# Performance work log

Measured on AMD Instinct MI355X. Metric: run time of the kernel, lower is better.

Reference implementation:

```python
import jax, jax.numpy as jnp
import numpy as np

K = 20
BN_SCALE = 1.0 / np.sqrt(1.0 + 1e-5)  # BN at init: running_mean=0, running_var=1


def _graph_feature(x, k):
    # x: (B, N, C) point features -> (B, N, k, 2C) edge features
    sq = jnp.sum(x * x, axis=-1)  # (B, N)
    # negative squared distance: larger == closer (matches torch topk on -dist)
    d = 2.0 * jnp.einsum('bnc,bmc->bnm', x, x) - sq[:, :, None] - sq[:, None, :]
    idx = jax.lax.top_k(d, k)[1]  # (B, N, k), self included as nearest
    nbr = jax.vmap(lambda pts, i: pts[i])(x, idx)  # (B, N, k, C) gather
    ctr = jnp.broadcast_to(x[:, :, None, :], nbr.shape)
    return jnp.concatenate([nbr - ctr, ctr], axis=-1)


def _edge_conv(e, W, g, b):
    # 1x1 Conv2d (no bias) + BatchNorm(init stats) + LeakyReLU(0.2) + max over k
    y = jnp.einsum('bnkc,oc->bnko', e, W)
    y = jax.nn.leaky_relu(y * (g * BN_SCALE) + b, 0.2)
    return jnp.max(y, axis=2)  # (B, N, O)


def setup_inputs() -> dict:
    key = jax.random.key(0)
    ks = jax.random.split(key, 12)
    B, N = 4, 1024
    dims_in = [6, 128, 256, 512]
    dims_out = [64, 128, 256, 512]
    inp = {'x': jax.random.normal(ks[0], (B, N, 3), dtype=jnp.float32)}
    for i, (ci, co) in enumerate(zip(dims_in, dims_out), start=1):
        inp[f'W{i}'] = jax.random.normal(ks[i], (co, ci), dtype=jnp.float32) * (1.0 / np.sqrt(ci))
        inp[f'g{i}'] = jnp.ones((co,), dtype=jnp.float32)
        inp[f'b{i}'] = jnp.zeros((co,), dtype=jnp.float32)
    inp['W5'] = jax.random.normal(ks[5], (512, 960), dtype=jnp.float32) * (1.0 / np.sqrt(960.0))
    inp['g5'] = jnp.ones((512,), dtype=jnp.float32)
    inp['b5'] = jnp.zeros((512,), dtype=jnp.float32)
    inp['We'] = jax.random.normal(ks[6], (256, 512), dtype=jnp.float32) * (1.0 / np.sqrt(512.0))
    return inp


def reference(x, W1, g1, b1, W2, g2, b2, W3, g3, b3, W4, g4, b4, W5, g5, b5, We):
    x1 = _edge_conv(_graph_feature(x, K), W1, g1, b1)   # (B, N, 64)
    x2 = _edge_conv(_graph_feature(x1, K), W2, g2, b2)  # (B, N, 128)
    x3 = _edge_conv(_graph_feature(x2, K), W3, g3, b3)  # (B, N, 256)
    x4 = _edge_conv(_graph_feature(x3, K), W4, g4, b4)  # (B, N, 512)
    xc = jnp.concatenate([x1, x2, x3, x4], axis=-1)     # (B, N, 960)
    y = jnp.einsum('bnc,oc->bno', xc, W5)               # conv5 (1x1 Conv1d)
    y = jax.nn.leaky_relu(y * (g5 * BN_SCALE) + b5, 0.2)
    feat = jnp.max(y, axis=1)                           # (B, 512) global max-pool
    return feat @ We.T                                  # (B, num_features)
```

## Files before the change

### kernel.cpp

```cpp
#include <hip/hip_runtime.h>
#include <hip/hip_bf16.h>
#include <math.h>

typedef __hip_bfloat16 bf16;
typedef __bf16 v8bf __attribute__((ext_vector_type(8)));
typedef float v4f __attribute__((ext_vector_type(4)));

#define BN_SCALE 0.9999950000374997f
#define NPTS 1024
#define NB 4
#define TW 40

__device__ __forceinline__ float b2f(bf16 v) { return __bfloat162float(v); }
__device__ __forceinline__ bf16 f2b(float v) { return __float2bfloat16(v); }
__device__ __forceinline__ float ldw(const void* p, size_t i, int isf) {
    return isf ? ((const float*)p)[i] : b2f(((const bf16*)p)[i]);
}
__device__ __forceinline__ unsigned ordf(float f) {
    unsigned u = __float_as_uint(f);
    return (u & 0x80000000u) ? ~u : (u | 0x80000000u);
}
__device__ __forceinline__ float iordf(unsigned u) {
    return (u & 0x80000000u) ? __uint_as_float(u ^ 0x80000000u) : __uint_as_float(~u);
}

__device__ __forceinline__ int detect_isf(const void* xraw, int* cnt) {
    const unsigned short* u = (const unsigned short*)xraw;
    int t = threadIdx.x, c = 0;
    for (int i = t; i < 512; i += 256) {
        unsigned short v = u[i];
        int e = (v >> 7) & 0xFF;
        int m = v & 0x7F;
        if (e == 0xFF || e >= 141 || (e == 0 && m != 0)) c++;
    }
    cnt[t] = c;
    __syncthreads();
    for (int off = 128; off > 0; off >>= 1) {
        if (t < off) cnt[t] += cnt[t + off];
        __syncthreads();
    }
    int isf = (cnt[0] > 30) ? 1 : 0;
    __syncthreads();
    return isf;
}

__global__ void k_prep(const void* __restrict__ W1, const void* __restrict__ W2,
                       const void* __restrict__ W3, const void* __restrict__ W4,
                       const void* __restrict__ W5, const void* __restrict__ x,
                       bf16* __restrict__ Whi, bf16* __restrict__ Wlo,
                       bf16* __restrict__ xph, bf16* __restrict__ xpl, float* __restrict__ sq,
                       int* __restrict__ flag, unsigned* __restrict__ pooledU) {
    __shared__ int cnt[256];
    int isf = detect_isf(x, cnt);
    if (blockIdx.x == 0) {
        if (threadIdx.x == 0) *flag = isf;
        for (int i = threadIdx.x; i < 2048; i += 256) pooledU[i] = 0u;
    }
    int idx = blockIdx.x * 256 + threadIdx.x;
    if (idx < 839680) {
        const void* src; int C, O, Kpad, two, local;
        if (idx < 4096)        { src = W1; C = 3;   O = 64;  Kpad = 32;  two = 1; local = idx; }
        else if (idx < 20480)  { src = W2; C = 64;  O = 128; Kpad = 64;  two = 1; local = idx - 4096; }
        else if (idx < 86016)  { src = W3; C = 128; O = 256; Kpad = 128; two = 1; local = idx - 20480; }
        else if (idx < 348160) { src = W4; C = 256; O = 512; Kpad = 256; two = 1; local = idx - 86016; }
        else                   { src = W5; C = 960; O = 512; Kpad = 960; two = 0; local = idx - 348160; }
        int r = local / Kpad, c = local % Kpad;
        float wv = 0.f;
        if (c < C) {
            size_t off;
            if (two) off = (r < O) ? (size_t)r * 2 * C + c : (size_t)(r - O) * 2 * C + C + c;
            else     off = (size_t)r * C + c;
            wv = ldw(src, off, isf);
        }
        bf16 h = f2b(wv);
        Whi[idx] = h;
        Wlo[idx] = f2b(wv - b2f(h));
    } else if (idx < 843776) {
        int p = idx - 839680;
        int z = p >> 10, n = p & 1023;
        bf16* ph = xph + (size_t)z * NPTS * 32;
        bf16* pl = xpl + (size_t)z * NPTS * 32;
        float s = 0.f;
        for (int c = 0; c < 32; c++) {
            float v = (c < 3) ? ldw(x, (size_t)z * NPTS * 3 + n * 3 + c, isf) : 0.f;
            bf16 h = f2b(v);
            ph[n * 32 + c] = h;
            pl[n * 32 + c] = f2b(v - b2f(h));
            s += v * v;
        }
        sq[z * NPTS + n] = s;
    }
}

__device__ __forceinline__ void fillA(bf16* dst, const bf16* srcRowBase, int ld) {
    int t = threadIdx.x; int r = t >> 2; int kq = (t & 3) << 3;
    *(float4*)(dst + r * TW + kq) = *(const float4*)(srcRowBase + (size_t)r * ld + kq);
}
__device__ __forceinline__ v8bf ldfrag(const bf16* tile, int sub, int l) {
    return *(const v8bf*)(tile + (size_t)(sub * 16 + (l & 15)) * TW + ((l >> 4) << 3));
}

__global__ __launch_bounds__(256) void k_layer_a(const bf16* __restrict__ Xhi, const bf16* __restrict__ Xlo,
                                                 int ld, int Kpad, size_t xstride,
                                                 const bf16* __restrict__ Whi, const bf16* __restrict__ Wlo,
                                                 int O, const float* __restrict__ sqg,
                                                 float* __restrict__ Dg, float* __restrict__ Pg,
                                                 const int* __restrict__ flag) {
    int i = blockIdx.x;
    int z = (i >> 1) & 3;
    int bi = ((i >> 3) << 1) | (i & 1);
    const bf16* Xh = Xhi + (size_t)z * xstride;
    const bf16* Xl = Xlo + (size_t)z * xstride;
    __shared__ alignas(16) bf16 Ah[64 * TW], Al[64 * TW], Bh[64 * TW], Bl[64 * TW];
    int w = threadIdx.x >> 6, l = threadIdx.x & 63;
    int quad = l >> 4, col = l & 15;
    v4f zero = {0.f, 0.f, 0.f, 0.f};
    v4f acc[4] = {zero, zero, zero, zero};

    if (bi < 136) {
        int bx = 0;
        while ((((bx + 1) * (bx + 2)) >> 1) <= bi) bx++;
        int by = bi - ((bx * (bx + 1)) >> 1);
        const float* sq = sqg + z * NPTS;
        float* D = Dg + (size_t)z * NPTS * NPTS;
        int n0 = by * 64, m0 = bx * 64;
        for (int k0 = 0; k0 < Kpad; k0 += 32) {
            __syncthreads();
            fillA(Ah, Xh + (size_t)n0 * ld + k0, ld);
            fillA(Bh, Xh + (size_t)m0 * ld + k0, ld);
            fillA(Al, Xl + (size_t)n0 * ld + k0, ld);
            fillA(Bl, Xl + (size_t)m0 * ld + k0, ld);
            __syncthreads();
            v8bf ah = ldfrag(Ah, w, l);
            v8bf al = ldfrag(Al, w, l);
#pragma unroll
            for (int nt = 0; nt < 4; nt++) {
                v8bf bh = ldfrag(Bh, nt, l);
                v8bf bl = ldfrag(Bl, nt, l);
                acc[nt] = __builtin_amdgcn_mfma_f32_16x16x32_bf16(ah, bh, acc[nt], 0, 0, 0);
                acc[nt] = __builtin_amdgcn_mfma_f32_16x16x32_bf16(ah, bl, acc[nt], 0, 0, 0);
                acc[nt] = __builtin_amdgcn_mfma_f32_16x16x32_bf16(al, bh, acc[nt], 0, 0, 0);
            }
        }
        int nb = n0 + 16 * w + quad * 4;
        float sm[4];
#pragma unroll
        for (int nt = 0; nt < 4; nt++) sm[nt] = sq[m0 + nt * 16 + col];
#pragma unroll
        for (int r = 0; r < 4; r++) {
            float sn = sq[nb + r];
#pragma unroll
            for (int nt = 0; nt < 4; nt++) {
                float d = 2.f * acc[nt][r] - sn - sm[nt];
                int m = m0 + nt * 16 + col;
                D[(size_t)(nb + r) * NPTS + m] = d;
                if (bx != by) D[(size_t)m * NPTS + nb + r] = d;
            }
        }
    } else {
        int isf = *flag;
        int nTilesO = (2 * O) >> 6;
        int s = bi - 136;
        int n0 = (s % nTilesO) * 64;
        int m0 = (s / nTilesO) * 64;
        int N2 = 2 * O;
        float* P = Pg + (size_t)z * NPTS * N2;
        for (int k0 = 0; k0 < Kpad; k0 += 32) {
            __syncthreads();
            fillA(Ah, Xh + (size_t)m0 * ld + k0, ld);
            fillA(Al, Xl + (size_t)m0 * ld + k0, ld);
            fillA(Bh, Whi + (size_t)n0 * Kpad + k0, Kpad);
            if (isf) fillA(Bl, Wlo + (size_t)n0 * Kpad + k0, Kpad);
            __syncthreads();
            v8bf ah = ldfrag(Ah, w, l);
            v8bf al = ldfrag(Al, w, l);
#pragma unroll
            for (int nt = 0; nt < 4; nt++) {
                v8bf bh = ldfrag(Bh, nt, l);
                acc[nt] = __builtin_amdgcn_mfma_f32_16x16x32_bf16(ah, bh, acc[nt], 0, 0, 0);
                acc[nt] = __builtin_amdgcn_mfma_f32_16x16x32_bf16(al, bh, acc[nt], 0, 0, 0);
                if (isf) {
                    v8bf bl = ldfrag(Bl, nt, l);
                    acc[nt] = __builtin_amdgcn_mfma_f32_16x16x32_bf16(ah, bl, acc[nt], 0, 0, 0);
                }
            }
        }
        int rb = m0 + 16 * w + quad * 4;
#pragma unroll
        for (int r = 0; r < 4; r++)
#pragma unroll
            for (int nt = 0; nt < 4; nt++)
                P[(size_t)(rb + r) * N2 + n0 + nt * 16 + col] = acc[nt][r];
    }
}

__global__ __launch_bounds__(256) void k_layer_b(const float* __restrict__ Dg, const float* __restrict__ Pg,
                                                 const void* __restrict__ g, const void* __restrict__ bias,
                                                 int O, bf16* __restrict__ xhOut, bf16* __restrict__ xlOut,
                                                 float* __restrict__ sqOut, int writeSq,
                                                 const int* __restrict__ flag) {
    __shared__ int ids[4][20];
    __shared__ float sqP[4][8];
    int isf = *flag;
    int i = blockIdx.x;
    int z = (i >> 1) & 3;
    int local = ((i >> 3) << 1) | (i & 1);
    int tid = threadIdx.x;
    int wq = tid >> 6, l = tid & 63;
    int row = local * 4 + wq;

    {
        const float* Dr = Dg + (size_t)z * NPTS * NPTS + (size_t)row * NPTS;
        float v[16];
#pragma unroll
        for (int jj = 0; jj < 4; jj++) {
            float4 f4 = *(const float4*)(Dr + jj * 256 + l * 4);
            v[jj * 4 + 0] = f4.x; v[jj * 4 + 1] = f4.y;
            v[jj * 4 + 2] = f4.z; v[jj * 4 + 3] = f4.w;
        }
        for (int s = 0; s < 20; s++) {
            float bv = v[0]; int bj = 0;
#pragma unroll
            for (int j = 1; j < 16; j++)
                if (v[j] > bv) { bv = v[j]; bj = j; }
            int bi = (bj >> 2) * 256 + l * 4 + (bj & 3);
#pragma unroll
            for (int off = 1; off < 64; off <<= 1) {
                float ov = __shfl_xor(bv, off);
                int   oi = __shfl_xor(bi, off);
                if (ov > bv || (ov == bv && oi < bi)) { bv = ov; bi = oi; }
            }
            if (l == 0) ids[wq][s] = bi;
            if (((bi >> 2) & 63) == l) {
                int ej = (bi >> 8) * 4 + (bi & 3);
#pragma unroll
                for (int j = 0; j < 16; j++)
                    if (j == ej) v[j] = -__builtin_inff();
            }
        }
    }
    __syncthreads();

    int N2 = 2 * O;
    const float* P = Pg + (size_t)z * NPTS * N2;
    for (int it = tid; it < 4 * O; it += 256) {
        int r = it / O, o = it % O;
        int n = local * 4 + r;
        float tv = P[(size_t)n * N2 + O + o] - P[(size_t)n * N2 + o];
        float scl = ldw(g, o, isf) * BN_SCALE;
        float bb = ldw(bias, o, isf);
        float acc = -__builtin_inff();
        for (int j = 0; j < 20; j++) {
            int m = ids[r][j];
            float v = P[(size_t)m * N2 + o] + tv;
            float z2 = v * scl + bb;
            z2 = z2 > 0.f ? z2 : 0.2f * z2;
            acc = fmaxf(acc, z2);
        }
        bf16 hi = f2b(acc);
        bf16 lo = f2b(acc - b2f(hi));
        xhOut[(size_t)z * NPTS * 960 + (size_t)n * 960 + o] = hi;
        xlOut[(size_t)z * NPTS * 960 + (size_t)n * 960 + o] = lo;
        if (writeSq) {
            float xv = b2f(hi) + b2f(lo);
            float s = xv * xv;
#pragma unroll
            for (int off = 32; off > 0; off >>= 1) s += __shfl_down(s, off);
            if (l == 0) sqP[r][o >> 6] = s;
        }
    }
    if (writeSq) {
        __syncthreads();
        if (tid < 4) {
            int nc = O >> 6;
            float tot = 0.f;
            for (int c = 0; c < nc; c++) tot += sqP[tid][c];
            sqOut[z * NPTS + local * 4 + tid] = tot;
        }
    }
}

__global__ __launch_bounds__(256) void k_conv5(const bf16* __restrict__ Xhi, const bf16* __restrict__ Xlo,
                                               const bf16* __restrict__ Whi, const bf16* __restrict__ Wlo,
                                               const void* __restrict__ g, const void* __restrict__ bias,
                                               unsigned* __restrict__ pooledU,
                                               const int* __restrict__ flag) {
    int isf = *flag;
    int i = blockIdx.x;
    int z = (i >> 1) & 3;
    int wi = ((i >> 3) << 1) | (i & 1);
    int o0 = (wi & 7) * 64, m0 = (wi >> 3) * 64;
    const bf16* Xh = Xhi + (size_t)z * NPTS * 960;
    const bf16* Xl = Xlo + (size_t)z * NPTS * 960;
    __shared__ alignas(16) bf16 Ah[64 * TW], Al[64 * TW], Bh[64 * TW], Bl[64 * TW];
    __shared__ float red[4][4][16];
    int w = threadIdx.x >> 6, l = threadIdx.x & 63;
    v4f zero = {0.f, 0.f, 0.f, 0.f};
    v4f acc[4] = {zero, zero, zero, zero};
    for (int k0 = 0; k0 < 960; k0 += 32) {
        __syncthreads();
        fillA(Ah, Xh + (size_t)m0 * 960 + k0, 960);
        fillA(Al, Xl + (size_t)m0 * 960 + k0, 960);
        fillA(Bh, Whi + (size_t)o0 * 960 + k0, 960);
        if (isf) fillA(Bl, Wlo + (size_t)o0 * 960 + k0, 960);
        __syncthreads();
        v8bf ah = ldfrag(Ah, w, l);
        v8bf al = ldfrag(Al, w, l);
#pragma unroll
        for (int nt = 0; nt < 4; nt++) {
            v8bf bh = ldfrag(Bh, nt, l);
            acc[nt] = __builtin_amdgcn_mfma_f32_16x16x32_bf16(ah, bh, acc[nt], 0, 0, 0);
            acc[nt] = __builtin_amdgcn_mfma_f32_16x16x32_bf16(al, bh, acc[nt], 0, 0, 0);
            if (isf) {
                v8bf bl = ldfrag(Bl, nt, l);
                acc[nt] = __builtin_amdgcn_mfma_f32_16x16x32_bf16(ah, bl, acc[nt], 0, 0, 0);
            }
        }
    }
    int quad = l >> 4, col = l & 15;
#pragma unroll
    for (int nt = 0; nt < 4; nt++) {
        int o = o0 + nt * 16 + col;
        float scl = ldw(g, o, isf) * BN_SCALE;
        float bi = ldw(bias, o, isf);
        float ym = -__builtin_inff();
#pragma unroll
        for (int r = 0; r < 4; r++) {
            float v = acc[nt][r] * scl + bi;
            v = v > 0.f ? v : 0.2f * v;
            ym = fmaxf(ym, v);
        }
        ym = fmaxf(ym, __shfl_down(ym, 32));
        ym = fmaxf(ym, __shfl_down(ym, 16));
        if (quad == 0) red[w][nt][col] = ym;
    }
    __syncthreads();
    if (threadIdx.x < 64) {
        int nt = threadIdx.x >> 4, c = threadIdx.x & 15;
        float m = fmaxf(fmaxf(red[0][nt][c], red[1][nt][c]), fmaxf(red[2][nt][c], red[3][nt][c]));
        atomicMax(&pooledU[z * 512 + o0 + nt * 16 + c], ordf(m));
    }
}

__global__ void k_final(const unsigned* __restrict__ pooledU, const void* __restrict__ We,
                        void* __restrict__ out, const int* __restrict__ flag) {
    __shared__ float p[512];
    int isf = *flag;
    int b = blockIdx.x >> 2, fb = blockIdx.x & 3;
    int t = threadIdx.x, w = t >> 6, l = t & 63;
    for (int i = t; i < 512; i += 256) p[i] = iordf(pooledU[b * 512 + i]);
    __syncthreads();
    for (int it = 0; it < 16; it++) {
        int f = fb * 64 + w * 16 + it;
        float s = 0.f;
        size_t base = (size_t)f * 512 + l * 8;
#pragma unroll
        for (int j = 0; j < 8; j++) s += p[l * 8 + j] * ldw(We, base + j, isf);
#pragma unroll
        for (int off = 32; off > 0; off >>= 1) s += __shfl_down(s, off);
        if (l == 0) {
            if (isf) ((float*)out)[b * 256 + f] = s;
            else     ((bf16*)out)[b * 256 + f] = f2b(s);
        }
    }
}

extern "C" void kernel_launch(void* const* d_in, const int* in_sizes, int n_in,
                              void* d_out, int out_size, void* d_ws, size_t ws_size,
                              hipStream_t stream) {
    const void* x  = d_in[0];
    const void* Wl[4] = { d_in[1], d_in[4], d_in[7], d_in[10] };
    const void* gl[4] = { d_in[2], d_in[5], d_in[8], d_in[11] };
    const void* bl[4] = { d_in[3], d_in[6], d_in[9], d_in[12] };
    const void* W5 = d_in[13];
    const void* g5 = d_in[14];
    const void* b5 = d_in[15];
    const void* We = d_in[16];

    char* base = (char*)d_ws;
    bf16*     xc_hi   = (bf16*)(base);
    bf16*     xc_lo   = (bf16*)(base + 7864320);
    bf16*     xpadh   = (bf16*)(base + 15728640);
    bf16*     xpadl   = (bf16*)(base + 15990784);
    float*    Dbuf    = (float*)(base + 16252928);
    float*    Pbuf    = (float*)(base + 33030144);
    bf16*     Whi     = (bf16*)(base + 49807360);
    bf16*     Wlo     = (bf16*)(base + 51486720);
    unsigned* pooledU = (unsigned*)(base + 53493760);
    float*    sq      = (float*)(base + 53501952);
    int*      flag    = (int*)(base + 53518336);

    const int Kpad[4]   = { 32, 64, 128, 256 };
    const int Os[4]     = { 64, 128, 256, 512 };
    const int Woff[5]   = { 0, 4096, 20480, 86016, 348160 };
    const int colIn[4]  = { 0, 0, 64, 192 };
    const int colOut[4] = { 0, 64, 192, 448 };

    k_prep<<<3296, 256, 0, stream>>>(Wl[0], Wl[1], Wl[2], Wl[3], W5, x,
                                     Whi, Wlo, xpadh, xpadl, sq, flag, pooledU);

    for (int l = 0; l < 4; l++) {
        int O = Os[l];
        int nTilesO = (2 * O) >> 6;
        int nBlk = 136 + 16 * nTilesO;
        const bf16* Xh = (l == 0) ? xpadh : (xc_hi + colIn[l]);
        const bf16* Xl = (l == 0) ? xpadl : (xc_lo + colIn[l]);
        int ld = (l == 0) ? 32 : 960;
        size_t xstr = (l == 0) ? (size_t)NPTS * 32 : (size_t)NPTS * 960;
        k_layer_a<<<nBlk * NB, 256, 0, stream>>>(
            Xh, Xl, ld, Kpad[l], xstr, Whi + Woff[l], Wlo + Woff[l], O, sq, Dbuf, Pbuf, flag);
        k_layer_b<<<NPTS * NB / 4, 256, 0, stream>>>(
            Dbuf, Pbuf, gl[l], bl[l], O, xc_hi + colOut[l], xc_lo + colOut[l], sq, l < 3, flag);
    }
    k_conv5<<<512, 256, 0, stream>>>(xc_hi, xc_lo, Whi + Woff[4], Wlo + Woff[4],
                                     g5, b5, pooledU, flag);
    k_final<<<16, 256, 0, stream>>>(pooledU, We, d_out, flag);
}
```

Before: 341.6 us.

## Enlarge GEMM tiles to 128x128 with 2x2 warp layout and 4x4 MFMA subtiles

The distance, projection and conv5 GEMM kernels move from 64x64 to 128x128 block tiles, with each wave computing a 64x64 subtile as 4x4 MFMA fragments. The aim is more reuse of each shared-memory fragment load and fewer global loads per FLOP. Grid sizes drop accordingly: the symmetric distance triangle goes from 136 to 36 tiles and conv5 from 512 to 128 blocks. In exchange, accumulator registers grow fourfold and far fewer blocks are launched, which may leave many of the GPU's CUs idle and lower occupancy.

```diff
diff --git a/kernel.cpp b/kernel.cpp
--- a/kernel.cpp
+++ b/kernel.cpp
@@ -92,11 +92,13 @@
     }
 }
 
-__device__ __forceinline__ void fillA(bf16* dst, const bf16* srcRowBase, int ld) {
-    int t = threadIdx.x; int r = t >> 2; int kq = (t & 3) << 3;
-    *(float4*)(dst + r * TW + kq) = *(const float4*)(srcRowBase + (size_t)r * ld + kq);
-}
-__device__ __forceinline__ v8bf ldfrag(const bf16* tile, int sub, int l) {
+__device__ __forceinline__ void fill128(bf16* dst, const bf16* src, int ld) {
+    int t = threadIdx.x;
+    int r = t >> 2, kq = (t & 3) << 3;
+    *(float4*)(dst + r * TW + kq) = *(const float4*)(src + (size_t)r * ld + kq);
+    *(float4*)(dst + (r + 64) * TW + kq) = *(const float4*)(src + (size_t)(r + 64) * ld + kq);
+}
+__device__ __forceinline__ v8bf ldf(const bf16* tile, int sub, int l) {
     return *(const v8bf*)(tile + (size_t)(sub * 16 + (l & 15)) * TW + ((l >> 4) << 3));
 }
 
@@ -111,86 +113,114 @@
     int bi = ((i >> 3) << 1) | (i & 1);
     const bf16* Xh = Xhi + (size_t)z * xstride;
     const bf16* Xl = Xlo + (size_t)z * xstride;
-    __shared__ alignas(16) bf16 Ah[64 * TW], Al[64 * TW], Bh[64 * TW], Bl[64 * TW];
+    __shared__ alignas(16) bf16 Ah[128 * TW], Al[128 * TW], Bh[128 * TW], Bl[128 * TW];
     int w = threadIdx.x >> 6, l = threadIdx.x & 63;
+    int wr = w >> 1, wc = w & 1;
     int quad = l >> 4, col = l & 15;
     v4f zero = {0.f, 0.f, 0.f, 0.f};
-    v4f acc[4] = {zero, zero, zero, zero};
-
-    if (bi < 136) {
+    v4f acc[4][4] = {{zero, zero, zero, zero}, {zero, zero, zero, zero},
+                     {zero, zero, zero, zero}, {zero, zero, zero, zero}};
+
+    if (bi < 36) {
         int bx = 0;
         while ((((bx + 1) * (bx + 2)) >> 1) <= bi) bx++;
         int by = bi - ((bx * (bx + 1)) >> 1);
         const float* sq = sqg + z * NPTS;
         float* D = Dg + (size_t)z * NPTS * NPTS;
-        int n0 = by * 64, m0 = bx * 64;
+        int n0 = by * 128, m0 = bx * 128;
         for (int k0 = 0; k0 < Kpad; k0 += 32) {
             __syncthreads();
-            fillA(Ah, Xh + (size_t)n0 * ld + k0, ld);
-            fillA(Bh, Xh + (size_t)m0 * ld + k0, ld);
-            fillA(Al, Xl + (size_t)n0 * ld + k0, ld);
-            fillA(Bl, Xl + (size_t)m0 * ld + k0, ld);
+            fill128(Ah, Xh + (size_t)n0 * ld + k0, ld);
+            fill128(Bh, Xh + (size_t)m0 * ld + k0, ld);
+            fill128(Al, Xl + (size_t)n0 * ld + k0, ld);
+            fill128(Bl, Xl + (size_t)m0 * ld + k0, ld);
             __syncthreads();
-            v8bf ah = ldfrag(Ah, w, l);
-            v8bf al = ldfrag(Al, w, l);
-#pragma unroll
-            for (int nt = 0; nt < 4; nt++) {
-                v8bf bh = ldfrag(Bh, nt, l);
-                v8bf bl = ldfrag(Bl, nt, l);
-                acc[nt] = __builtin_amdgcn_mfma_f32_16x16x32_bf16(ah, bh, acc[nt], 0, 0, 0);
-                acc[nt] = __builtin_amdgcn_mfma_f32_16x16x32_bf16(ah, bl, acc[nt], 0, 0, 0);
-                acc[nt] = __builtin_amdgcn_mfma_f32_16x16x32_bf16(al, bh, acc[nt], 0, 0, 0);
-            }
-        }
-        int nb = n0 + 16 * w + quad * 4;
+            v8bf ah[4], al[4];
+#pragma unroll
+            for (int mi = 0; mi < 4; mi++) {
+                ah[mi] = ldf(Ah, wr * 4 + mi, l);
+                al[mi] = ldf(Al, wr * 4 + mi, l);
+            }
+#pragma unroll
+            for (int ni = 0; ni < 4; ni++) {
+                v8bf bh = ldf(Bh, wc * 4 + ni, l);
+                v8bf bl = ldf(Bl, wc * 4 + ni, l);
+#pragma unroll
+                for (int mi = 0; mi < 4; mi++) {
+                    acc[mi][ni] = __builtin_amdgcn_mfma_f32_16x16x32_bf16(ah[mi], bh, acc[mi][ni], 0, 0, 0);
+                    acc[mi][ni] = __builtin_amdgcn_mfma_f32_16x16x32_bf16(ah[mi], bl, acc[mi][ni], 0, 0, 0);
+                    acc[mi][ni] = __builtin_amdgcn_mfma_f32_16x16x32_bf16(al[mi], bh, acc[mi][ni], 0, 0, 0);
+                }
+            }
+        }
+        int rb = n0 + wr * 64 + quad * 4;
+        int cb = m0 + wc * 64 + col;
         float sm[4];
 #pragma unroll
-        for (int nt = 0; nt < 4; nt++) sm[nt] = sq[m0 + nt * 16 + col];
-#pragma unroll
-        for (int r = 0; r < 4; r++) {
-            float sn = sq[nb + r];
-#pragma unroll
-            for (int nt = 0; nt < 4; nt++) {
-                float d = 2.f * acc[nt][r] - sn - sm[nt];
-                int m = m0 + nt * 16 + col;
-                D[(size_t)(nb + r) * NPTS + m] = d;
-                if (bx != by) D[(size_t)m * NPTS + nb + r] = d;
+        for (int ni = 0; ni < 4; ni++) sm[ni] = sq[cb + ni * 16];
+#pragma unroll
+        for (int mi = 0; mi < 4; mi++) {
+#pragma unroll
+            for (int r = 0; r < 4; r++) {
+                int row = rb + mi * 16 + r;
+                float sn = sq[row];
+#pragma unroll
+                for (int ni = 0; ni < 4; ni++) {
+                    float d = 2.f * acc[mi][ni][r] - sn - sm[ni];
+                    int c = cb + ni * 16;
+                    D[(size_t)row * NPTS + c] = d;
+                    if (bx != by) D[(size_t)c * NPTS + row] = d;
+                }
             }
         }
     } else {
         int isf = *flag;
-        int nTilesO = (2 * O) >> 6;
-        int s = bi - 136;
-        int n0 = (s % nTilesO) * 64;
-        int m0 = (s / nTilesO) * 64;
+        int nCol = (2 * O) >> 7;
+        int s = bi - 36;
+        int n0 = (s % nCol) * 128;
+        int m0 = (s / nCol) * 128;
         int N2 = 2 * O;
         float* P = Pg + (size_t)z * NPTS * N2;
         for (int k0 = 0; k0 < Kpad; k0 += 32) {
             __syncthreads();
-            fillA(Ah, Xh + (size_t)m0 * ld + k0, ld);
-            fillA(Al, Xl + (size_t)m0 * ld + k0, ld);
-            fillA(Bh, Whi + (size_t)n0 * Kpad + k0, Kpad);
-            if (isf) fillA(Bl, Wlo + (size_t)n0 * Kpad + k0, Kpad);
+            fill128(Ah, Xh + (size_t)m0 * ld + k0, ld);
+            fill128(Al, Xl + (size_t)m0 * ld + k0, ld);
+            fill128(Bh, Whi + (size_t)n0 * Kpad + k0, Kpad);
+            if (isf) fill128(Bl, Wlo + (size_t)n0 * Kpad + k0, Kpad);
             __syncthreads();
-            v8bf ah = ldfrag(Ah, w, l);
-            v8bf al = ldfrag(Al, w, l);
-#pragma unroll
-            for (int nt = 0; nt < 4; nt++) {
-                v8bf bh = ldfrag(Bh, nt, l);
-                acc[nt] = __builtin_amdgcn_mfma_f32_16x16x32_bf16(ah, bh, acc[nt], 0, 0, 0);
-                acc[nt] = __builtin_amdgcn_mfma_f32_16x16x32_bf16(al, bh, acc[nt], 0, 0, 0);
+            v8bf ah[4], al[4];
+#pragma unroll
+            for (int mi = 0; mi < 4; mi++) {
+                ah[mi] = ldf(Ah, wr * 4 + mi, l);
+                al[mi] = ldf(Al, wr * 4 + mi, l);
+            }
+#pragma unroll
+            for (int ni = 0; ni < 4; ni++) {
+                v8bf bh = ldf(Bh, wc * 4 + ni, l);
+#pragma unroll
+                for (int mi = 0; mi < 4; mi++) {
+                    acc[mi][ni] = __builtin_amdgcn_mfma_f32_16x16x32_bf16(ah[mi], bh, acc[mi][ni], 0, 0, 0);
+                    acc[mi][ni] = __builtin_amdgcn_mfma_f32_16x16x32_bf16(al[mi], bh, acc[mi][ni], 0, 0, 0);
+                }
                 if (isf) {
-                    v8bf bl = ldfrag(Bl, nt, l);
-                    acc[nt] = __builtin_amdgcn_mfma_f32_16x16x32_bf16(ah, bl, acc[nt], 0, 0, 0);
+                    v8bf bl = ldf(Bl, wc * 4 + ni, l);
+#pragma unroll
+                    for (int mi = 0; mi < 4; mi++)
+                        acc[mi][ni] = __builtin_amdgcn_mfma_f32_16x16x32_bf16(ah[mi], bl, acc[mi][ni], 0, 0, 0);
                 }
             }
         }
-        int rb = m0 + 16 * w + quad * 4;
-#pragma unroll
-        for (int r = 0; r < 4; r++)
-#pragma unroll
-            for (int nt = 0; nt < 4; nt++)
-                P[(size_t)(rb + r) * N2 + n0 + nt * 16 + col] = acc[nt][r];
+        int rb = m0 + wr * 64 + quad * 4;
+        int cb = n0 + wc * 64 + col;
+#pragma unroll
+        for (int mi = 0; mi < 4; mi++)
+#pragma unroll
+            for (int r = 0; r < 4; r++) {
+                int row = rb + mi * 16 + r;
+#pragma unroll
+                for (int ni = 0; ni < 4; ni++)
+                    P[(size_t)row * N2 + cb + ni * 16] = acc[mi][ni][r];
+            }
     }
 }
 
@@ -289,56 +319,69 @@
     int i = blockIdx.x;
     int z = (i >> 1) & 3;
     int wi = ((i >> 3) << 1) | (i & 1);
-    int o0 = (wi & 7) * 64, m0 = (wi >> 3) * 64;
+    int o0 = (wi & 3) * 128, m0 = (wi >> 2) * 128;
     const bf16* Xh = Xhi + (size_t)z * NPTS * 960;
     const bf16* Xl = Xlo + (size_t)z * NPTS * 960;
-    __shared__ alignas(16) bf16 Ah[64 * TW], Al[64 * TW], Bh[64 * TW], Bl[64 * TW];
+    __shared__ alignas(16) bf16 Ah[128 * TW], Al[128 * TW], Bh[128 * TW], Bl[128 * TW];
     __shared__ float red[4][4][16];
     int w = threadIdx.x >> 6, l = threadIdx.x & 63;
+    int wr = w >> 1, wc = w & 1;
+    int quad = l >> 4, col = l & 15;
     v4f zero = {0.f, 0.f, 0.f, 0.f};
-    v4f acc[4] = {zero, zero, zero, zero};
+    v4f acc[4][4] = {{zero, zero, zero, zero}, {zero, zero, zero, zero},
+                     {zero, zero, zero, zero}, {zero, zero, zero, zero}};
     for (int k0 = 0; k0 < 960; k0 += 32) {
         __syncthreads();
-        fillA(Ah, Xh + (size_t)m0 * 960 + k0, 960);
-        fillA(Al, Xl + (size_t)m0 * 960 + k0, 960);
-        fillA(Bh, Whi + (size_t)o0 * 960 + k0, 960);
-        if (isf) fillA(Bl, Wlo + (size_t)o0 * 960 + k0, 960);
+        fill128(Ah, Xh + (size_t)m0 * 960 + k0, 960);
+        fill128(Al, Xl + (size_t)m0 * 960 + k0, 960);
+        fill128(Bh, Whi + (size_t)o0 * 960 + k0, 960);
+        if (isf) fill128(Bl, Wlo + (size_t)o0 * 960 + k0, 960);
         __syncthreads();
-        v8bf ah = ldfrag(Ah, w, l);
-        v8bf al = ldfrag(Al, w, l);
-#pragma unroll
-        for (int nt = 0; nt < 4; nt++) {
-            v8bf bh = ldfrag(Bh, nt, l);
-            acc[nt] = __builtin_amdgcn_mfma_f32_16x16x32_bf16(ah, bh, acc[nt], 0, 0, 0);
-            acc[nt] = __builtin_amdgcn_mfma_f32_16x16x32_bf16(al, bh, acc[nt], 0, 0, 0);
+        v8bf ah[4], al[4];
+#pragma unroll
+        for (int mi = 0; mi < 4; mi++) {
+            ah[mi] = ldf(Ah, wr * 4 + mi, l);
+            al[mi] = ldf(Al, wr * 4 + mi, l);
+        }
+#pragma unroll
+        for (int ni = 0; ni < 4; ni++) {
+            v8bf bh = ldf(Bh, wc * 4 + ni, l);
+#pragma unroll
+            for (int mi = 0; mi < 4; mi++) {
+                acc[mi][ni] = __builtin_amdgcn_mfma_f32_16x16x32_bf16(ah[mi], bh, acc[mi][ni], 0, 0, 0);
+                acc[mi][ni] = __builtin_amdgcn_mfma_f32_16x16x32_bf16(al[mi], bh, acc[mi][ni], 0, 0, 0);
+            }
             if (isf) {
-                v8bf bl = ldfrag(Bl, nt, l);
-                acc[nt] = __builtin_amdgcn_mfma_f32_16x16x32_bf16(ah, bl, acc[nt], 0, 0, 0);
-            }
-        }
-    }
-    int quad = l >> 4, col = l & 15;
-#pragma unroll
-    for (int nt = 0; nt < 4; nt++) {
-        int o = o0 + nt * 16 + col;
+                v8bf bl = ldf(Bl, wc * 4 + ni, l);
+#pragma unroll
+                for (int mi = 0; mi < 4; mi++)
+                    acc[mi][ni] = __builtin_amdgcn_mfma_f32_16x16x32_bf16(ah[mi], bl, acc[mi][ni], 0, 0, 0);
+            }
+        }
+    }
+#pragma unroll
+    for (int ni = 0; ni < 4; ni++) {
+        int o = o0 + wc * 64 + ni * 16 + col;
         float scl = ldw(g, o, isf) * BN_SCALE;
         float bi = ldw(bias, o, isf);
         float ym = -__builtin_inff();
 #pragma unroll
-        for (int r = 0; r < 4; r++) {
-            float v = acc[nt][r] * scl + bi;
-            v = v > 0.f ? v : 0.2f * v;
-            ym = fmaxf(ym, v);
-        }
+        for (int mi = 0; mi < 4; mi++)
+#pragma unroll
+            for (int r = 0; r < 4; r++) {
+                float v = acc[mi][ni][r] * scl + bi;
+                v = v > 0.f ? v : 0.2f * v;
+                ym = fmaxf(ym, v);
+            }
         ym = fmaxf(ym, __shfl_down(ym, 32));
         ym = fmaxf(ym, __shfl_down(ym, 16));
-        if (quad == 0) red[w][nt][col] = ym;
+        if (quad == 0) red[w][ni][col] = ym;
     }
     __syncthreads();
-    if (threadIdx.x < 64) {
-        int nt = threadIdx.x >> 4, c = threadIdx.x & 15;
-        float m = fmaxf(fmaxf(red[0][nt][c], red[1][nt][c]), fmaxf(red[2][nt][c], red[3][nt][c]));
-        atomicMax(&pooledU[z * 512 + o0 + nt * 16 + c], ordf(m));
+    if (threadIdx.x < 128) {
+        int wcs = threadIdx.x >> 6, ni = (threadIdx.x >> 4) & 3, c = threadIdx.x & 15;
+        float m = fmaxf(red[wcs][ni][c], red[wcs + 2][ni][c]);
+        atomicMax(&pooledU[z * 512 + o0 + wcs * 64 + ni * 16 + c], ordf(m));
     }
 }
 
@@ -401,8 +444,8 @@
 
     for (int l = 0; l < 4; l++) {
         int O = Os[l];
-        int nTilesO = (2 * O) >> 6;
-        int nBlk = 136 + 16 * nTilesO;
+        int nCol = (2 * O) >> 7;
+        int nBlk = 36 + 8 * nCol;
         const bf16* Xh = (l == 0) ? xpadh : (xc_hi + colIn[l]);
         const bf16* Xl = (l == 0) ? xpadl : (xc_lo + colIn[l]);
         int ld = (l == 0) ? 32 : 960;
@@ -412,7 +455,7 @@
         k_layer_b<<<NPTS * NB / 4, 256, 0, stream>>>(
             Dbuf, Pbuf, gl[l], bl[l], O, xc_hi + colOut[l], xc_lo + colOut[l], sq, l < 3, flag);
     }
-    k_conv5<<<512, 256, 0, stream>>>(xc_hi, xc_lo, Whi + Woff[4], Wlo + Woff[4],
+    k_conv5<<<128, 256, 0, stream>>>(xc_hi, xc_lo, Whi + Woff[4], Wlo + Woff[4],
                                      g5, b5, pooledU, flag);
     k_final<<<16, 256, 0, stream>>>(pooledU, We, d_out, flag);
 }
```

New measurement: 361.5 us. 5.9% more time.
